# Performance work log

Hardware: AMD Instinct MI355X
Metric: run time of the kernel (lower is better)

The kernel has to match this reference:

```python
import jax, jax.numpy as jnp
import numpy as np

HEADS = 4
DIM_HEAD = 32
CHUNK = 1024
GROUPS = 8
EPS = 1e-5


def setup_inputs() -> dict:
    key = jax.random.key(0)
    k1, k2, k3 = jax.random.split(key, 3)
    b, dim, h, w = 8, 64, 96, 96
    inner = HEADS * DIM_HEAD  # 128
    x = jax.random.normal(k1, (b, dim, h, w), dtype=jnp.float32)
    W_qkv = jax.random.normal(k2, (3 * inner, dim), dtype=jnp.float32) * (1.0 / np.sqrt(dim))
    W_out = jax.random.normal(k3, (dim, inner), dtype=jnp.float32) * (1.0 / np.sqrt(inner))
    b_out = jnp.zeros((dim,), dtype=jnp.float32)
    gamma = jnp.ones((dim,), dtype=jnp.float32)
    beta = jnp.zeros((dim,), dtype=jnp.float32)
    return {"x": x, "W_qkv": W_qkv, "W_out": W_out, "b_out": b_out,
            "gamma": gamma, "beta": beta}


def reference(x, W_qkv, W_out, b_out, gamma, beta):
    b, c, h, w = x.shape
    n = h * w
    nch = n // CHUNK  # number of full chunks (n chosen divisible by CHUNK)
    d = DIM_HEAD
    BH = b * HEADS

    # 1x1 conv (no bias) == matmul over channel dim
    xf = x.reshape(b, c, n)
    qkv = jnp.einsum('oc,bcn->bon', W_qkv, xf)          # [b, 3*inner, n]
    q, k, v = jnp.split(qkv, 3, axis=1)                  # each [b, inner, n]

    def chunkify(t):
        # [b, inner, n] -> [BH, nch, d, CHUNK]; slicing i:i+CHUNK on last axis
        # equals reshaping n -> (nch, CHUNK) in order.
        return t.reshape(BH, d, nch, CHUNK).transpose(0, 2, 1, 3)

    qc, kc, vc = chunkify(q), chunkify(k), chunkify(v)

    qs = jax.nn.softmax(qc, axis=-1)  # softmax over chunk spatial positions
    ks = jax.nn.softmax(kc, axis=-2)  # softmax over head channels

    # context = k_chunk^T @ v_chunk : [BH, nch, CHUNK, CHUNK]
    ctx = jnp.einsum('gkdi,gkdj->gkij', ks, vc)
    # chunk_out = q_chunk @ context : [BH, nch, d, CHUNK]
    out = jnp.einsum('gkdi,gkij->gkdj', qs, ctx)

    # concat chunks back along spatial dim, reshape to image layout
    out = out.transpose(0, 2, 1, 3).reshape(b, HEADS * d, h, w)

    # to_out: 1x1 conv with bias, then GroupNorm(8, dim)
    y = jnp.einsum('oc,bchw->bohw', W_out, out) + b_out[None, :, None, None]

    yg = y.reshape(b, GROUPS, c // GROUPS, h, w)
    mu = jnp.mean(yg, axis=(2, 3, 4), keepdims=True)
    var = jnp.var(yg, axis=(2, 3, 4), keepdims=True)
    yn = ((yg - mu) * jax.lax.rsqrt(var + EPS)).reshape(b, c, h, w)
    return yn * gamma[None, :, None, None] + beta[None, :, None, None]
```

## Files before the change

kernel.cpp:

```cpp
#include <hip/hip_runtime.h>
#include <hip/hip_bf16.h>

#define N_POS 9216
#define NCHUNK 9
#define CHUNKN 1024
#define BATCH 8
#define CDIM 64
#define HEADS 4
#define GROUPS 8
#define EPS 1e-5f

#define SEC_SZ ((size_t)BATCH * N_POS * 128)
#define QKV_BYTES (3 * SEC_SZ * 2)
#define PPART_SZ ((size_t)32 * NCHUNK * 1024)

typedef __attribute__((ext_vector_type(8))) short short8;
typedef __attribute__((ext_vector_type(4))) float f32x4;

static __device__ inline unsigned pk2(float a, float b) {
    __hip_bfloat162 h2(__float2bfloat16(a), __float2bfloat16(b));
    return *reinterpret_cast<unsigned*>(&h2);
}
static __device__ inline float bf2f(short s) {
    union { unsigned u; float f; } c; c.u = ((unsigned)(unsigned short)s) << 16; return c.f;
}

__global__ __launch_bounds__(256) void qkv_kernel(const float* __restrict__ x,
        const float* __restrict__ Wqkv, __hip_bfloat16* __restrict__ qkv) {
    int n0  = blockIdx.x * 256;
    int sec = blockIdx.y;
    int b   = blockIdx.z;
    __shared__ __align__(16) char lds_raw[256 * 136 * 2];
    __hip_bfloat16 (*xs)[72]    = (__hip_bfloat16(*)[72])lds_raw;
    __hip_bfloat16 (*wsm)[72]   = (__hip_bfloat16(*)[72])(lds_raw + 256*72*2);
    __hip_bfloat16 (*vbuf)[136] = (__hip_bfloat16(*)[136])lds_raw;
    int t = threadIdx.x;
    int w = t >> 6, l = t & 63;

    {
        const float* xb = x + (size_t)b * CDIM * N_POS + n0 + t;
        #pragma unroll
        for (int c = 0; c < 64; c += 4) {
            float v0 = xb[(size_t)(c + 0) * N_POS];
            float v1 = xb[(size_t)(c + 1) * N_POS];
            float v2 = xb[(size_t)(c + 2) * N_POS];
            float v3 = xb[(size_t)(c + 3) * N_POS];
            uint2 u; u.x = pk2(v0, v1); u.y = pk2(v2, v3);
            *reinterpret_cast<uint2*>(&xs[t][c]) = u;
        }
    }
    {
        int m = t >> 1, ch = (t & 1) * 32;
        const float4* wr = (const float4*)(Wqkv + ((size_t)sec * 128 + m) * CDIM + ch);
        #pragma unroll
        for (int j = 0; j < 8; ++j) {
            float4 v = wr[j];
            uint2 u; u.x = pk2(v.x, v.y); u.y = pk2(v.z, v.w);
            *reinterpret_cast<uint2*>(&wsm[m][ch + j * 4]) = u;
        }
    }
    __syncthreads();

    int lrow = l & 15, lquad = l >> 4;
    f32x4 acc[8][4];
    #pragma unroll
    for (int mt = 0; mt < 8; ++mt)
        #pragma unroll
        for (int nt = 0; nt < 4; ++nt) acc[mt][nt] = (f32x4){0.f, 0.f, 0.f, 0.f};

    #pragma unroll
    for (int ks = 0; ks < 2; ++ks) {
        int k0 = lquad * 8 + ks * 32;
        short8 bfr[4];
        #pragma unroll
        for (int nt = 0; nt < 4; ++nt) {
            int n = w * 64 + nt * 16 + lrow;
            bfr[nt] = *reinterpret_cast<const short8*>(&xs[n][k0]);
        }
        #pragma unroll
        for (int mt = 0; mt < 8; ++mt) {
            short8 afr = *reinterpret_cast<const short8*>(&wsm[mt * 16 + lrow][k0]);
            #pragma unroll
            for (int nt = 0; nt < 4; ++nt)
                acc[mt][nt] = __builtin_amdgcn_mfma_f32_16x16x32_bf16(afr, bfr[nt], acc[mt][nt], 0, 0, 0);
        }
    }
    __syncthreads();

    #pragma unroll
    for (int mt = 0; mt < 8; ++mt)
        #pragma unroll
        for (int nt = 0; nt < 4; ++nt) {
            int n = w * 64 + nt * 16 + lrow;
            uint2 u;
            u.x = pk2(acc[mt][nt][0], acc[mt][nt][1]);
            u.y = pk2(acc[mt][nt][2], acc[mt][nt][3]);
            *reinterpret_cast<uint2*>(&vbuf[n][mt * 16 + lquad * 4]) = u;
        }
    __syncthreads();

    __hip_bfloat16* outb = qkv + (size_t)sec * SEC_SZ + ((size_t)b * N_POS + n0) * 128;
    int rg = t >> 4, c0 = (t & 15) * 8;
    #pragma unroll
    for (int j = 0; j < 16; ++j) {
        int r = j * 16 + rg;
        *reinterpret_cast<uint4*>(outb + (size_t)r * 128 + c0) =
            *reinterpret_cast<const uint4*>(&vbuf[r][c0]);
    }
}

__global__ __launch_bounds__(256) void smat_part(const __hip_bfloat16* __restrict__ qkv,
        float* __restrict__ Pparts) {
    int bh = blockIdx.x, ck = blockIdx.y, pt = blockIdx.z;
    int b = bh >> 2, h = bh & 3;
    int p = ck * CHUNKN + pt * 256 + threadIdx.x;
    __shared__ __hip_bfloat16 qsb[32][264];
    __shared__ __hip_bfloat16 ksb[32][264];
    int t = threadIdx.x, w = t >> 6, l = t & 63;
    const __hip_bfloat16* qp = qkv + ((size_t)b * N_POS + p) * 128 + h * 32;
    const __hip_bfloat16* kp = qkv + SEC_SZ + ((size_t)b * N_POS + p) * 128 + h * 32;
    {
        short8 kv4[4];
        #pragma unroll
        for (int j = 0; j < 4; ++j) kv4[j] = *reinterpret_cast<const short8*>(kp + j * 8);
        float kr[32]; float mx = -1e30f;
        #pragma unroll
        for (int j = 0; j < 4; ++j)
            #pragma unroll
            for (int e = 0; e < 8; ++e) { kr[j*8+e] = bf2f(kv4[j][e]); mx = fmaxf(mx, kr[j*8+e]); }
        float s = 0.f;
        #pragma unroll
        for (int d = 0; d < 32; ++d) { kr[d] = __expf(kr[d] - mx); s += kr[d]; }
        float is = 1.f / s;
        #pragma unroll
        for (int d = 0; d < 32; ++d) ksb[d][t] = __float2bfloat16(kr[d] * is);
    }
    {
        short8 qv4[4];
        #pragma unroll
        for (int j = 0; j < 4; ++j) qv4[j] = *reinterpret_cast<const short8*>(qp + j * 8);
        #pragma unroll
        for (int j = 0; j < 4; ++j)
            #pragma unroll
            for (int e = 0; e < 8; ++e)
                qsb[j*8+e][t] = __float2bfloat16(__expf(bf2f(qv4[j][e])));
    }
    __syncthreads();

    int mt = w >> 1, nt = w & 1;
    int l15 = l & 15, quad = l >> 4;
    f32x4 acc = (f32x4){0.f, 0.f, 0.f, 0.f};
    #pragma unroll
    for (int step = 0; step < 8; ++step) {
        int k0 = step * 32 + quad * 8;
        short8 af = *reinterpret_cast<const short8*>(&qsb[mt * 16 + l15][k0]);
        short8 bf = *reinterpret_cast<const short8*>(&ksb[nt * 16 + l15][k0]);
        acc = __builtin_amdgcn_mfma_f32_16x16x32_bf16(af, bf, acc, 0, 0, 0);
    }
    float* Pp = Pparts + (size_t)pt * PPART_SZ + ((size_t)bh * NCHUNK + ck) * 1024;
    #pragma unroll
    for (int r = 0; r < 4; ++r)
        Pp[(mt * 16 + quad * 4 + r) * 32 + nt * 16 + l15] = acc[r];
}

__global__ __launch_bounds__(256) void umat_kernel(const float* __restrict__ Wout,
        const float* __restrict__ Pparts, __hip_bfloat16* __restrict__ Ubf,
        float* __restrict__ stats) {
    int ck = blockIdx.x, b = blockIdx.y, h = blockIdx.z;
    int bh = b * 4 + h;
    int t = threadIdx.x;
    if (ck == 0 && h == 0 && t < 16) stats[b * 16 + t] = 0.f;
    __shared__ float Pl[32][32];
    __shared__ float iZ[32];
    size_t base4 = (((size_t)bh * NCHUNK + ck) * 1024) / 4;
    {
        const float4* P0 = (const float4*)Pparts + base4;
        const float4* P1 = (const float4*)(Pparts + PPART_SZ) + base4;
        const float4* P2 = (const float4*)(Pparts + 2 * PPART_SZ) + base4;
        const float4* P3 = (const float4*)(Pparts + 3 * PPART_SZ) + base4;
        float4 a = P0[t], bb = P1[t], c = P2[t], d = P3[t];
        float4 s; s.x = a.x+bb.x+c.x+d.x; s.y = a.y+bb.y+c.y+d.y;
        s.z = a.z+bb.z+c.z+d.z; s.w = a.w+bb.w+c.w+d.w;
        ((float4*)Pl)[t] = s;
    }
    __syncthreads();
    if (t < 32) {
        float s = 0.f;
        #pragma unroll
        for (int c = 0; c < 32; ++c) s += Pl[t][c];
        iZ[t] = 1.f / s;
    }
    __syncthreads();
    int o = t & 63, wv = t >> 6;
    float wz[32];
    {
        const float4* wr = (const float4*)(Wout + (size_t)o * 128 + h * 32);
        #pragma unroll
        for (int j = 0; j < 8; ++j) {
            float4 f = wr[j];
            wz[j*4+0] = f.x * iZ[j*4+0]; wz[j*4+1] = f.y * iZ[j*4+1];
            wz[j*4+2] = f.z * iZ[j*4+2]; wz[j*4+3] = f.w * iZ[j*4+3];
        }
    }
    float ua[8];
    #pragma unroll
    for (int j = 0; j < 8; ++j) ua[j] = 0.f;
    for (int d = 0; d < 32; ++d) {
        float wd = wz[d];
        #pragma unroll
        for (int j = 0; j < 8; ++j) ua[j] += wd * Pl[d][wv * 8 + j];
    }
    uint4 up;
    up.x = pk2(ua[0], ua[1]); up.y = pk2(ua[2], ua[3]);
    up.z = pk2(ua[4], ua[5]); up.w = pk2(ua[6], ua[7]);
    __hip_bfloat16* Up = Ubf + ((size_t)(b * NCHUNK + ck) * 64 + o) * 128 + h * 32 + wv * 8;
    *reinterpret_cast<uint4*>(Up) = up;
}

__global__ __launch_bounds__(256) void y_kernel(const __hip_bfloat16* __restrict__ qkv,
        const __hip_bfloat16* __restrict__ Ubf, const float* __restrict__ bout,
        float* __restrict__ y, float* __restrict__ stats) {
    int bx = blockIdx.x;
    int b  = blockIdx.y;
    int ck = bx >> 3;
    __shared__ float gsum[8], gsq[8];
    int t = threadIdx.x, w = t >> 6, l = t & 63;
    int l15 = l & 15, quad = l >> 4;
    if (t < 8) { gsum[t] = 0.f; gsq[t] = 0.f; }
    __syncthreads();
    const __hip_bfloat16* vt = qkv + 2 * SEC_SZ + (size_t)b * N_POS * 128;
    const __hip_bfloat16* Ub = Ubf + (size_t)(b * NCHUNK + ck) * 64 * 128;
    int nbase = bx * 128 + w * 32;
    f32x4 acc[4][2];
    #pragma unroll
    for (int mt = 0; mt < 4; ++mt) { acc[mt][0] = (f32x4){0,0,0,0}; acc[mt][1] = (f32x4){0,0,0,0}; }
    #pragma unroll
    for (int ks = 0; ks < 4; ++ks) {
        int k0 = ks * 32 + quad * 8;
        short8 bf[2];
        #pragma unroll
        for (int nt = 0; nt < 2; ++nt)
            bf[nt] = *reinterpret_cast<const short8*>(vt + (size_t)(nbase + nt * 16 + l15) * 128 + k0);
        #pragma unroll
        for (int mt = 0; mt < 4; ++mt) {
            short8 af = *reinterpret_cast<const short8*>(Ub + (size_t)(mt * 16 + l15) * 128 + k0);
            acc[mt][0] = __builtin_amdgcn_mfma_f32_16x16x32_bf16(af, bf[0], acc[mt][0], 0, 0, 0);
            acc[mt][1] = __builtin_amdgcn_mfma_f32_16x16x32_bf16(af, bf[1], acc[mt][1], 0, 0, 0);
        }
    }
    float gsl[4], gql[4];
    #pragma unroll
    for (int mt = 0; mt < 4; ++mt) { gsl[mt] = 0.f; gql[mt] = 0.f; }
    float* yb = y + (size_t)b * CDIM * N_POS;
    #pragma unroll
    for (int mt = 0; mt < 4; ++mt) {
        float4 bo = *reinterpret_cast<const float4*>(bout + mt * 16 + quad * 4);
        const float* bop = reinterpret_cast<const float*>(&bo);
        #pragma unroll
        for (int nt = 0; nt < 2; ++nt) {
            int n = nbase + nt * 16 + l15;
            #pragma unroll
            for (int r = 0; r < 4; ++r) {
                int o = mt * 16 + quad * 4 + r;
                float val = acc[mt][nt][r] + bop[r];
                yb[(size_t)o * N_POS + n] = val;
                gsl[mt] += val; gql[mt] += val * val;
            }
        }
    }
    #pragma unroll
    for (int off = 16; off >= 1; off >>= 1) {
        #pragma unroll
        for (int mt = 0; mt < 4; ++mt) {
            gsl[mt] += __shfl_xor(gsl[mt], off, 64);
            gql[mt] += __shfl_xor(gql[mt], off, 64);
        }
    }
    if (l == 0 || l == 32) {
        int qh = quad >> 1;
        #pragma unroll
        for (int mt = 0; mt < 4; ++mt) {
            atomicAdd(&gsum[2 * mt + qh], gsl[mt]);
            atomicAdd(&gsq[2 * mt + qh], gql[mt]);
        }
    }
    __syncthreads();
    if (t < 8) {
        atomicAdd(&stats[(b * 8 + t) * 2],     gsum[t]);
        atomicAdd(&stats[(b * 8 + t) * 2 + 1], gsq[t]);
    }
}

__global__ __launch_bounds__(256) void gn_kernel(float* __restrict__ y,
        const float* __restrict__ stats, const float* __restrict__ gamma,
        const float* __restrict__ beta) {
    int i4 = blockIdx.x * 256 + threadIdx.x;
    if (i4 >= (BATCH * CDIM * N_POS) / 4) return;
    int base = i4 * 4;
    int bc = base / N_POS;
    int c = bc & 63, b = bc >> 6;
    int g = c >> 3;
    float s = stats[(b * 8 + g) * 2], q = stats[(b * 8 + g) * 2 + 1];
    const float invN = 1.f / (8.f * N_POS);
    float mean = s * invN;
    float var = q * invN - mean * mean;
    float sc = rsqrtf(var + EPS);
    float ga = gamma[c] * sc;
    float be = beta[c] - mean * sc * gamma[c];
    float4 v = ((float4*)y)[i4];
    v.x = v.x * ga + be; v.y = v.y * ga + be; v.z = v.z * ga + be; v.w = v.w * ga + be;
    ((float4*)y)[i4] = v;
}

extern "C" void kernel_launch(void* const* d_in, const int* in_sizes, int n_in,
                              void* d_out, int out_size, void* d_ws, size_t ws_size,
                              hipStream_t stream) {
    const float* x     = (const float*)d_in[0];
    const float* Wqkv  = (const float*)d_in[1];
    const float* Wout  = (const float*)d_in[2];
    const float* bout  = (const float*)d_in[3];
    const float* gamma = (const float*)d_in[4];
    const float* beta  = (const float*)d_in[5];
    float* out = (float*)d_out;

    __hip_bfloat16* qkv = (__hip_bfloat16*)d_ws;
    float* stats  = (float*)((char*)d_ws + QKV_BYTES);
    float* Pparts = stats + 128;
    __hip_bfloat16* Ubf = (__hip_bfloat16*)(Pparts + 4 * PPART_SZ);

    qkv_kernel<<<dim3(36, 3, BATCH), 256, 0, stream>>>(x, Wqkv, qkv);
    smat_part<<<dim3(32, NCHUNK, 4), 256, 0, stream>>>(qkv, Pparts);
    umat_kernel<<<dim3(NCHUNK, BATCH, HEADS), 256, 0, stream>>>(Wout, Pparts, Ubf, stats);
    y_kernel<<<dim3(72, BATCH), 256, 0, stream>>>(qkv, Ubf, bout, out, stats);
    gn_kernel<<<dim3((BATCH * CDIM * N_POS / 4 + 255) / 256), 256, 0, stream>>>(out, stats, gamma, beta);
}
```

Before: 133.2 us.

## Fuse Q/K projection with softmax and QK^T partials, drop Q/K workspace

Replaces the separate QKV projection and smat_part kernels with a fused qkp_kernel. It computes Q and K for a 64-position tile in LDS, applies the softmaxes, and directly emits per-tile 32x32 partial products, split 16 ways per chunk. V is still projected by its own kernel into workspace. This removes the write and re-read of the bf16 Q and K tensors through global memory. In exchange, each block reloads the x tile separately for the fused and V kernels, and umat must reduce 16 partials instead of 4.

```diff
diff --git a/kernel.cpp b/kernel.cpp
--- a/kernel.cpp
+++ b/kernel.cpp
@@ -10,9 +10,10 @@
 #define GROUPS 8
 #define EPS 1e-5f
 
-#define SEC_SZ ((size_t)BATCH * N_POS * 128)
-#define QKV_BYTES (3 * SEC_SZ * 2)
+#define VSEC_SZ ((size_t)BATCH * N_POS * 128)
+#define VSEC_BYTES (VSEC_SZ * 2)
 #define PPART_SZ ((size_t)32 * NCHUNK * 1024)
+#define NPART 16
 
 typedef __attribute__((ext_vector_type(8))) short short8;
 typedef __attribute__((ext_vector_type(4))) float f32x4;
@@ -25,142 +26,198 @@
     union { unsigned u; float f; } c; c.u = ((unsigned)(unsigned short)s) << 16; return c.f;
 }
 
-__global__ __launch_bounds__(256) void qkv_kernel(const float* __restrict__ x,
-        const float* __restrict__ Wqkv, __hip_bfloat16* __restrict__ qkv) {
-    int n0  = blockIdx.x * 256;
-    int sec = blockIdx.y;
-    int b   = blockIdx.z;
-    __shared__ __align__(16) char lds_raw[256 * 136 * 2];
-    __hip_bfloat16 (*xs)[72]    = (__hip_bfloat16(*)[72])lds_raw;
-    __hip_bfloat16 (*wsm)[72]   = (__hip_bfloat16(*)[72])(lds_raw + 256*72*2);
-    __hip_bfloat16 (*vbuf)[136] = (__hip_bfloat16(*)[136])lds_raw;
-    int t = threadIdx.x;
-    int w = t >> 6, l = t & 63;
-
-    {
-        const float* xb = x + (size_t)b * CDIM * N_POS + n0 + t;
-        #pragma unroll
-        for (int c = 0; c < 64; c += 4) {
-            float v0 = xb[(size_t)(c + 0) * N_POS];
-            float v1 = xb[(size_t)(c + 1) * N_POS];
-            float v2 = xb[(size_t)(c + 2) * N_POS];
-            float v3 = xb[(size_t)(c + 3) * N_POS];
+__global__ __launch_bounds__(256) void qkp_kernel(const float* __restrict__ x,
+        const float* __restrict__ Wqkv, float* __restrict__ Pparts) {
+    int bx = blockIdx.x;
+    int b  = blockIdx.y;
+    int ck = bx >> 4, pt = bx & 15;
+    int n0 = bx * 64;
+    __shared__ __align__(16) char lraw[46080];
+    __hip_bfloat16 (*xs)[72]  = (__hip_bfloat16(*)[72])lraw;
+    __hip_bfloat16 (*wsm)[72] = (__hip_bfloat16(*)[72])(lraw + 9216);
+    __hip_bfloat16 (*skT)[72] = (__hip_bfloat16(*)[72])lraw;
+    int t = threadIdx.x, w = t >> 6, l = t & 63;
+    int l15 = l & 15, quad = l >> 4;
+
+    {
+        int p = t & 63, cbase = (t >> 6) * 16;
+        const float* xb = x + (size_t)b * CDIM * N_POS + n0 + p;
+        #pragma unroll
+        for (int j = 0; j < 16; j += 4) {
+            float v0 = xb[(size_t)(cbase + j + 0) * N_POS];
+            float v1 = xb[(size_t)(cbase + j + 1) * N_POS];
+            float v2 = xb[(size_t)(cbase + j + 2) * N_POS];
+            float v3 = xb[(size_t)(cbase + j + 3) * N_POS];
             uint2 u; u.x = pk2(v0, v1); u.y = pk2(v2, v3);
-            *reinterpret_cast<uint2*>(&xs[t][c]) = u;
-        }
-    }
-    {
-        int m = t >> 1, ch = (t & 1) * 32;
-        const float4* wr = (const float4*)(Wqkv + ((size_t)sec * 128 + m) * CDIM + ch);
+            *reinterpret_cast<uint2*>(&xs[p][cbase + j]) = u;
+        }
+    }
+    {
+        const float4* wr = (const float4*)Wqkv;
+        #pragma unroll
+        for (int j = 0; j < 16; ++j) {
+            int f = t + j * 256;
+            float4 v = wr[f];
+            uint2 u; u.x = pk2(v.x, v.y); u.y = pk2(v.z, v.w);
+            *reinterpret_cast<uint2*>(&wsm[f >> 4][(f & 15) * 4]) = u;
+        }
+    }
+    __syncthreads();
+
+    int mbase = (w >> 1) * 128;
+    int nh = (w & 1) * 32;
+    f32x4 acc[8][2];
+    #pragma unroll
+    for (int mt = 0; mt < 8; ++mt) { acc[mt][0] = (f32x4){0,0,0,0}; acc[mt][1] = (f32x4){0,0,0,0}; }
+    #pragma unroll
+    for (int ks = 0; ks < 2; ++ks) {
+        int k0 = ks * 32 + quad * 8;
+        short8 bfr[2];
+        #pragma unroll
+        for (int nt = 0; nt < 2; ++nt)
+            bfr[nt] = *reinterpret_cast<const short8*>(&xs[nh + nt * 16 + l15][k0]);
+        #pragma unroll
+        for (int mt = 0; mt < 8; ++mt) {
+            short8 afr = *reinterpret_cast<const short8*>(&wsm[mbase + mt * 16 + l15][k0]);
+            acc[mt][0] = __builtin_amdgcn_mfma_f32_16x16x32_bf16(afr, bfr[0], acc[mt][0], 0, 0, 0);
+            acc[mt][1] = __builtin_amdgcn_mfma_f32_16x16x32_bf16(afr, bfr[1], acc[mt][1], 0, 0, 0);
+        }
+    }
+    __syncthreads();
+
+    #pragma unroll
+    for (int mt = 0; mt < 8; ++mt)
+        #pragma unroll
+        for (int nt = 0; nt < 2; ++nt) {
+            int p = nh + nt * 16 + l15;
+            #pragma unroll
+            for (int r = 0; r < 4; ++r)
+                skT[mbase + mt * 16 + quad * 4 + r][p] = __float2bfloat16(acc[mt][nt][r]);
+        }
+    __syncthreads();
+
+    {
+        int p = t & 63, h = t >> 6;
+        float kr[32]; float mx = -1e30f;
+        #pragma unroll
+        for (int d = 0; d < 32; ++d) { kr[d] = bf2f(*(const short*)&skT[128 + h * 32 + d][p]); mx = fmaxf(mx, kr[d]); }
+        float s = 0.f;
+        #pragma unroll
+        for (int d = 0; d < 32; ++d) { kr[d] = __expf(kr[d] - mx); s += kr[d]; }
+        float is = 1.f / s;
+        #pragma unroll
+        for (int d = 0; d < 32; ++d) skT[128 + h * 32 + d][p] = __float2bfloat16(kr[d] * is);
+        #pragma unroll
+        for (int d = 0; d < 32; ++d) {
+            float qv = bf2f(*(const short*)&skT[h * 32 + d][p]);
+            skT[h * 32 + d][p] = __float2bfloat16(__expf(qv));
+        }
+    }
+    __syncthreads();
+
+    f32x4 pac[2][2];
+    pac[0][0] = (f32x4){0,0,0,0}; pac[0][1] = (f32x4){0,0,0,0};
+    pac[1][0] = (f32x4){0,0,0,0}; pac[1][1] = (f32x4){0,0,0,0};
+    #pragma unroll
+    for (int step = 0; step < 2; ++step) {
+        int k0 = step * 32 + quad * 8;
+        short8 bk[2];
+        #pragma unroll
+        for (int nt = 0; nt < 2; ++nt)
+            bk[nt] = *reinterpret_cast<const short8*>(&skT[128 + w * 32 + nt * 16 + l15][k0]);
+        #pragma unroll
+        for (int mt = 0; mt < 2; ++mt) {
+            short8 aq = *reinterpret_cast<const short8*>(&skT[w * 32 + mt * 16 + l15][k0]);
+            pac[mt][0] = __builtin_amdgcn_mfma_f32_16x16x32_bf16(aq, bk[0], pac[mt][0], 0, 0, 0);
+            pac[mt][1] = __builtin_amdgcn_mfma_f32_16x16x32_bf16(aq, bk[1], pac[mt][1], 0, 0, 0);
+        }
+    }
+    float* Pp = Pparts + (size_t)pt * PPART_SZ + ((size_t)(b * 4 + w) * NCHUNK + ck) * 1024;
+    #pragma unroll
+    for (int mt = 0; mt < 2; ++mt)
+        #pragma unroll
+        for (int nt = 0; nt < 2; ++nt)
+            #pragma unroll
+            for (int r = 0; r < 4; ++r)
+                Pp[(mt * 16 + quad * 4 + r) * 32 + nt * 16 + l15] = pac[mt][nt][r];
+}
+
+__global__ __launch_bounds__(256) void v_kernel(const float* __restrict__ x,
+        const float* __restrict__ Wqkv, __hip_bfloat16* __restrict__ vsec) {
+    int n0 = blockIdx.x * 128;
+    int b  = blockIdx.y;
+    __shared__ __align__(16) char lraw[36864];
+    __hip_bfloat16 (*xs)[72]    = (__hip_bfloat16(*)[72])lraw;
+    __hip_bfloat16 (*wsm)[72]   = (__hip_bfloat16(*)[72])(lraw + 18432);
+    __hip_bfloat16 (*vbuf)[136] = (__hip_bfloat16(*)[136])lraw;
+    int t = threadIdx.x, w = t >> 6, l = t & 63;
+    int l15 = l & 15, quad = l >> 4;
+
+    {
+        int p = t & 127, cbase = (t >> 7) * 32;
+        const float* xb = x + (size_t)b * CDIM * N_POS + n0 + p;
+        #pragma unroll
+        for (int j = 0; j < 32; j += 4) {
+            float v0 = xb[(size_t)(cbase + j + 0) * N_POS];
+            float v1 = xb[(size_t)(cbase + j + 1) * N_POS];
+            float v2 = xb[(size_t)(cbase + j + 2) * N_POS];
+            float v3 = xb[(size_t)(cbase + j + 3) * N_POS];
+            uint2 u; u.x = pk2(v0, v1); u.y = pk2(v2, v3);
+            *reinterpret_cast<uint2*>(&xs[p][cbase + j]) = u;
+        }
+    }
+    {
+        const float4* wr = (const float4*)(Wqkv + 256 * CDIM);
         #pragma unroll
         for (int j = 0; j < 8; ++j) {
-            float4 v = wr[j];
+            int f = t + j * 256;
+            float4 v = wr[f];
             uint2 u; u.x = pk2(v.x, v.y); u.y = pk2(v.z, v.w);
-            *reinterpret_cast<uint2*>(&wsm[m][ch + j * 4]) = u;
-        }
-    }
-    __syncthreads();
-
-    int lrow = l & 15, lquad = l >> 4;
-    f32x4 acc[8][4];
+            *reinterpret_cast<uint2*>(&wsm[f >> 4][(f & 15) * 4]) = u;
+        }
+    }
+    __syncthreads();
+
+    int nw = w * 32;
+    f32x4 acc[8][2];
+    #pragma unroll
+    for (int mt = 0; mt < 8; ++mt) { acc[mt][0] = (f32x4){0,0,0,0}; acc[mt][1] = (f32x4){0,0,0,0}; }
+    #pragma unroll
+    for (int ks = 0; ks < 2; ++ks) {
+        int k0 = ks * 32 + quad * 8;
+        short8 bfr[2];
+        #pragma unroll
+        for (int nt = 0; nt < 2; ++nt)
+            bfr[nt] = *reinterpret_cast<const short8*>(&xs[nw + nt * 16 + l15][k0]);
+        #pragma unroll
+        for (int mt = 0; mt < 8; ++mt) {
+            short8 afr = *reinterpret_cast<const short8*>(&wsm[mt * 16 + l15][k0]);
+            acc[mt][0] = __builtin_amdgcn_mfma_f32_16x16x32_bf16(afr, bfr[0], acc[mt][0], 0, 0, 0);
+            acc[mt][1] = __builtin_amdgcn_mfma_f32_16x16x32_bf16(afr, bfr[1], acc[mt][1], 0, 0, 0);
+        }
+    }
+    __syncthreads();
+
     #pragma unroll
     for (int mt = 0; mt < 8; ++mt)
         #pragma unroll
-        for (int nt = 0; nt < 4; ++nt) acc[mt][nt] = (f32x4){0.f, 0.f, 0.f, 0.f};
-
-    #pragma unroll
-    for (int ks = 0; ks < 2; ++ks) {
-        int k0 = lquad * 8 + ks * 32;
-        short8 bfr[4];
-        #pragma unroll
-        for (int nt = 0; nt < 4; ++nt) {
-            int n = w * 64 + nt * 16 + lrow;
-            bfr[nt] = *reinterpret_cast<const short8*>(&xs[n][k0]);
-        }
-        #pragma unroll
-        for (int mt = 0; mt < 8; ++mt) {
-            short8 afr = *reinterpret_cast<const short8*>(&wsm[mt * 16 + lrow][k0]);
-            #pragma unroll
-            for (int nt = 0; nt < 4; ++nt)
-                acc[mt][nt] = __builtin_amdgcn_mfma_f32_16x16x32_bf16(afr, bfr[nt], acc[mt][nt], 0, 0, 0);
-        }
-    }
-    __syncthreads();
-
-    #pragma unroll
-    for (int mt = 0; mt < 8; ++mt)
-        #pragma unroll
-        for (int nt = 0; nt < 4; ++nt) {
-            int n = w * 64 + nt * 16 + lrow;
+        for (int nt = 0; nt < 2; ++nt) {
+            int p = nw + nt * 16 + l15;
             uint2 u;
             u.x = pk2(acc[mt][nt][0], acc[mt][nt][1]);
             u.y = pk2(acc[mt][nt][2], acc[mt][nt][3]);
-            *reinterpret_cast<uint2*>(&vbuf[n][mt * 16 + lquad * 4]) = u;
-        }
-    __syncthreads();
-
-    __hip_bfloat16* outb = qkv + (size_t)sec * SEC_SZ + ((size_t)b * N_POS + n0) * 128;
+            *reinterpret_cast<uint2*>(&vbuf[p][mt * 16 + quad * 4]) = u;
+        }
+    __syncthreads();
+
+    __hip_bfloat16* outb = vsec + ((size_t)b * N_POS + n0) * 128;
     int rg = t >> 4, c0 = (t & 15) * 8;
     #pragma unroll
-    for (int j = 0; j < 16; ++j) {
+    for (int j = 0; j < 8; ++j) {
         int r = j * 16 + rg;
         *reinterpret_cast<uint4*>(outb + (size_t)r * 128 + c0) =
             *reinterpret_cast<const uint4*>(&vbuf[r][c0]);
     }
-}
-
-__global__ __launch_bounds__(256) void smat_part(const __hip_bfloat16* __restrict__ qkv,
-        float* __restrict__ Pparts) {
-    int bh = blockIdx.x, ck = blockIdx.y, pt = blockIdx.z;
-    int b = bh >> 2, h = bh & 3;
-    int p = ck * CHUNKN + pt * 256 + threadIdx.x;
-    __shared__ __hip_bfloat16 qsb[32][264];
-    __shared__ __hip_bfloat16 ksb[32][264];
-    int t = threadIdx.x, w = t >> 6, l = t & 63;
-    const __hip_bfloat16* qp = qkv + ((size_t)b * N_POS + p) * 128 + h * 32;
-    const __hip_bfloat16* kp = qkv + SEC_SZ + ((size_t)b * N_POS + p) * 128 + h * 32;
-    {
-        short8 kv4[4];
-        #pragma unroll
-        for (int j = 0; j < 4; ++j) kv4[j] = *reinterpret_cast<const short8*>(kp + j * 8);
-        float kr[32]; float mx = -1e30f;
-        #pragma unroll
-        for (int j = 0; j < 4; ++j)
-            #pragma unroll
-            for (int e = 0; e < 8; ++e) { kr[j*8+e] = bf2f(kv4[j][e]); mx = fmaxf(mx, kr[j*8+e]); }
-        float s = 0.f;
-        #pragma unroll
-        for (int d = 0; d < 32; ++d) { kr[d] = __expf(kr[d] - mx); s += kr[d]; }
-        float is = 1.f / s;
-        #pragma unroll
-        for (int d = 0; d < 32; ++d) ksb[d][t] = __float2bfloat16(kr[d] * is);
-    }
-    {
-        short8 qv4[4];
-        #pragma unroll
-        for (int j = 0; j < 4; ++j) qv4[j] = *reinterpret_cast<const short8*>(qp + j * 8);
-        #pragma unroll
-        for (int j = 0; j < 4; ++j)
-            #pragma unroll
-            for (int e = 0; e < 8; ++e)
-                qsb[j*8+e][t] = __float2bfloat16(__expf(bf2f(qv4[j][e])));
-    }
-    __syncthreads();
-
-    int mt = w >> 1, nt = w & 1;
-    int l15 = l & 15, quad = l >> 4;
-    f32x4 acc = (f32x4){0.f, 0.f, 0.f, 0.f};
-    #pragma unroll
-    for (int step = 0; step < 8; ++step) {
-        int k0 = step * 32 + quad * 8;
-        short8 af = *reinterpret_cast<const short8*>(&qsb[mt * 16 + l15][k0]);
-        short8 bf = *reinterpret_cast<const short8*>(&ksb[nt * 16 + l15][k0]);
-        acc = __builtin_amdgcn_mfma_f32_16x16x32_bf16(af, bf, acc, 0, 0, 0);
-    }
-    float* Pp = Pparts + (size_t)pt * PPART_SZ + ((size_t)bh * NCHUNK + ck) * 1024;
-    #pragma unroll
-    for (int r = 0; r < 4; ++r)
-        Pp[(mt * 16 + quad * 4 + r) * 32 + nt * 16 + l15] = acc[r];
 }
 
 __global__ __launch_bounds__(256) void umat_kernel(const float* __restrict__ Wout,
@@ -172,15 +229,15 @@
     if (ck == 0 && h == 0 && t < 16) stats[b * 16 + t] = 0.f;
     __shared__ float Pl[32][32];
     __shared__ float iZ[32];
-    size_t base4 = (((size_t)bh * NCHUNK + ck) * 1024) / 4;
-    {
-        const float4* P0 = (const float4*)Pparts + base4;
-        const float4* P1 = (const float4*)(Pparts + PPART_SZ) + base4;
-        const float4* P2 = (const float4*)(Pparts + 2 * PPART_SZ) + base4;
-        const float4* P3 = (const float4*)(Pparts + 3 * PPART_SZ) + base4;
-        float4 a = P0[t], bb = P1[t], c = P2[t], d = P3[t];
-        float4 s; s.x = a.x+bb.x+c.x+d.x; s.y = a.y+bb.y+c.y+d.y;
-        s.z = a.z+bb.z+c.z+d.z; s.w = a.w+bb.w+c.w+d.w;
+    size_t base4 = ((size_t)bh * NCHUNK + ck) * 256;
+    {
+        const float4* P0 = (const float4*)Pparts + base4 + t;
+        float4 s = (float4){0.f, 0.f, 0.f, 0.f};
+        #pragma unroll
+        for (int j = 0; j < NPART; ++j) {
+            float4 a = P0[j * (PPART_SZ / 4)];
+            s.x += a.x; s.y += a.y; s.z += a.z; s.w += a.w;
+        }
         ((float4*)Pl)[t] = s;
     }
     __syncthreads();
@@ -217,7 +274,7 @@
     *reinterpret_cast<uint4*>(Up) = up;
 }
 
-__global__ __launch_bounds__(256) void y_kernel(const __hip_bfloat16* __restrict__ qkv,
+__global__ __launch_bounds__(256) void y_kernel(const __hip_bfloat16* __restrict__ vsec,
         const __hip_bfloat16* __restrict__ Ubf, const float* __restrict__ bout,
         float* __restrict__ y, float* __restrict__ stats) {
     int bx = blockIdx.x;
@@ -228,7 +285,7 @@
     int l15 = l & 15, quad = l >> 4;
     if (t < 8) { gsum[t] = 0.f; gsq[t] = 0.f; }
     __syncthreads();
-    const __hip_bfloat16* vt = qkv + 2 * SEC_SZ + (size_t)b * N_POS * 128;
+    const __hip_bfloat16* vt = vsec + (size_t)b * N_POS * 128;
     const __hip_bfloat16* Ub = Ubf + (size_t)(b * NCHUNK + ck) * 64 * 128;
     int nbase = bx * 128 + w * 32;
     f32x4 acc[4][2];
@@ -323,14 +380,14 @@
     const float* beta  = (const float*)d_in[5];
     float* out = (float*)d_out;
 
-    __hip_bfloat16* qkv = (__hip_bfloat16*)d_ws;
-    float* stats  = (float*)((char*)d_ws + QKV_BYTES);
+    __hip_bfloat16* vsec = (__hip_bfloat16*)d_ws;
+    float* stats  = (float*)((char*)d_ws + VSEC_BYTES);
     float* Pparts = stats + 128;
-    __hip_bfloat16* Ubf = (__hip_bfloat16*)(Pparts + 4 * PPART_SZ);
-
-    qkv_kernel<<<dim3(36, 3, BATCH), 256, 0, stream>>>(x, Wqkv, qkv);
-    smat_part<<<dim3(32, NCHUNK, 4), 256, 0, stream>>>(qkv, Pparts);
+    __hip_bfloat16* Ubf = (__hip_bfloat16*)(Pparts + NPART * PPART_SZ);
+
+    qkp_kernel<<<dim3(144, BATCH), 256, 0, stream>>>(x, Wqkv, Pparts);
+    v_kernel<<<dim3(72, BATCH), 256, 0, stream>>>(x, Wqkv, vsec);
     umat_kernel<<<dim3(NCHUNK, BATCH, HEADS), 256, 0, stream>>>(Wout, Pparts, Ubf, stats);
-    y_kernel<<<dim3(72, BATCH), 256, 0, stream>>>(qkv, Ubf, bout, out, stats);
+    y_kernel<<<dim3(72, BATCH), 256, 0, stream>>>(vsec, Ubf, bout, out, stats);
     gn_kernel<<<dim3((BATCH * CDIM * N_POS / 4 + 255) / 256), 256, 0, stream>>>(out, stats, gamma, beta);
 }
```

After: 127.9 us. -4.0%, faster.
